# Kernel optimization log

Measured on AMD Instinct MI355X. Metric: run time of the kernel, lower is better.

Reference implementation:

```python
import jax, jax.numpy as jnp
import numpy as np

N = 10000   # nodes
E = 320000  # edges
D = 3000    # input genes
H1, H2 = 1024, 128
F1, F2, F3, F4 = 256, 512, 1024, 2048
BN_EPS = 1e-5

def setup_inputs() -> dict:
    key = jax.random.key(0)
    ks = jax.random.split(key, 30)
    rn = lambda k, s, sc=0.05: jax.random.normal(k, s, dtype=jnp.float32) * sc
    inp = {}
    inp["x"] = jax.random.normal(ks[0], (N, D), dtype=jnp.float32)
    inp["edge_w"] = jax.random.uniform(ks[1], (E,), dtype=jnp.float32)
    inp["W1"] = rn(ks[2], (D, H1))
    inp["W2"] = rn(ks[3], (H1, H2))
    inp["W3"] = rn(ks[4], (H1, H2))
    dims = [(H2, F1), (F1, F2), (F2, F3), (F3, F4), (F4, D)]
    for i, (di, do) in enumerate(dims, start=1):
        inp[f"fc{i}_w"] = rn(ks[4 + i], (di, do))
        inp[f"fc{i}_b"] = jnp.zeros((do,), jnp.float32)
        if i <= 4:
            inp[f"bn{i}_g"] = jnp.ones((do,), jnp.float32)
            inp[f"bn{i}_b"] = jnp.zeros((do,), jnp.float32)
    inp["edge_src"] = jax.random.randint(ks[20], (E,), 0, N)
    inp["edge_dst"] = jax.random.randint(ks[21], (E,), 0, N)
    return inp

def reference(x, edge_w, W1, W2, W3,
              fc1_w, fc1_b, bn1_g, bn1_b,
              fc2_w, fc2_b, bn2_g, bn2_b,
              fc3_w, fc3_b, bn3_g, bn3_b,
              fc4_w, fc4_b, bn4_g, bn4_b,
              fc5_w, fc5_b, edge_src, edge_dst):
    # sparse adjacency matmul: out[dst] += w * h[src]
    def spmm(h):
        return jax.ops.segment_sum(h[edge_src] * edge_w[:, None], edge_dst, num_segments=N)
    # GCN encoder: GraphConvolution = act(adj @ (x @ W)) (dropout inactive in eval)
    h1 = jax.nn.relu(spmm(x @ W1))
    mu = spmm(h1 @ W2)
    logvar = spmm(h1 @ W3)
    z = mu  # eval-mode reparameterize returns mu
    # inner-product adjacency decoder (act = identity)
    adj_rec = z @ z.T
    # FC stack: Linear -> BatchNorm(eval, running mean=0, var=1) -> ReLU
    inv = 1.0 / jnp.sqrt(jnp.float32(1.0 + BN_EPS))
    def fc(h, w, b, g, be):
        return jax.nn.relu((h @ w + b) * inv * g + be)
    o = fc(z, fc1_w, fc1_b, bn1_g, bn1_b)
    o = fc(o, fc2_w, fc2_b, bn2_g, bn2_b)
    o = fc(o, fc3_w, fc3_b, bn3_g, bn3_b)
    o = fc(o, fc4_w, fc4_b, bn4_g, bn4_b)
    x_rec = o @ fc5_w + fc5_b  # fc5: no batchnorm, identity act
    return (adj_rec, mu, logvar, z, x_rec)
```

## Files before the change

### kernel.cpp

```cpp
#include <hip/hip_runtime.h>
#include <stdint.h>

typedef unsigned short ushort_t;
typedef __attribute__((ext_vector_type(8))) short short8;
typedef __attribute__((ext_vector_type(4))) float f32x4;

#define N_NODES 10000
#define MP      10240
#define E_EDGES 320000
#define D_IN    3000
#define K1P     3008
#define H1      1024
#define H2      128

static __device__ __forceinline__ float b2f(ushort_t u) {
  union { uint32_t u; float f; } x; x.u = ((uint32_t)u) << 16; return x.f;
}
static __device__ __forceinline__ ushort_t f2b(float f) {
  union { float f; uint32_t u; } x; x.f = f;
  uint32_t r = x.u + 0x7FFF + ((x.u >> 16) & 1);
  return (ushort_t)(r >> 16);
}

static __device__ __forceinline__ void gload16(const void* g, void* l) {
  __builtin_amdgcn_global_load_lds(
      (const __attribute__((address_space(1))) uint32_t*)g,
      (__attribute__((address_space(3))) uint32_t*)l, 16, 0, 0);
}

__global__ void zero_k(int* p, int n) {
  int i = blockIdx.x * 256 + threadIdx.x;
  if (i < n) p[i] = 0;
}
__global__ void count_k(const int* __restrict__ ed, int* __restrict__ cnt) {
  int e = blockIdx.x * 256 + threadIdx.x;
  if (e < E_EDGES) atomicAdd(&cnt[ed[e]], 1);
}
__global__ void scan_k(const int* __restrict__ cnt, int* __restrict__ rs, int* __restrict__ cur) {
  __shared__ int sums[256];
  int t = threadIdx.x;
  const int per = 40;
  int base = t * per;
  int s = 0;
  for (int i = 0; i < per; i++) { int idx = base + i; if (idx < N_NODES) s += cnt[idx]; }
  sums[t] = s;
  __syncthreads();
  if (t == 0) { int run = 0; for (int i = 0; i < 256; i++) { int v = sums[i]; sums[i] = run; run += v; } }
  __syncthreads();
  int run = sums[t];
  for (int i = 0; i < per; i++) {
    int idx = base + i;
    if (idx < N_NODES) { rs[idx] = run; cur[idx] = run; run += cnt[idx]; }
  }
  if (t == 255) rs[N_NODES] = run;
}
__global__ void fill_k(const int* __restrict__ es, const int* __restrict__ ed,
                       const float* __restrict__ ew,
                       int* __restrict__ cur, int* __restrict__ psrc, float* __restrict__ pw) {
  int e = blockIdx.x * 256 + threadIdx.x;
  if (e >= E_EDGES) return;
  int d = ed[e];
  int pos = atomicAdd(&cur[d], 1);
  psrc[pos] = es[e];
  pw[pos] = ew[e];
}

__global__ void conv_x_k(const float* __restrict__ x, ushort_t* __restrict__ xb) {
  int g = blockIdx.x * 256 + threadIdx.x;
  int row = g / 376;
  int c8 = (g % 376) * 8;
  float v[8];
  if (row < N_NODES && c8 < 3000) {
    const float4 f0 = *(const float4*)(x + (size_t)row * 3000 + c8);
    const float4 f1 = *(const float4*)(x + (size_t)row * 3000 + c8 + 4);
    v[0]=f0.x; v[1]=f0.y; v[2]=f0.z; v[3]=f0.w;
    v[4]=f1.x; v[5]=f1.y; v[6]=f1.z; v[7]=f1.w;
  } else {
#pragma unroll
    for (int i = 0; i < 8; i++) v[i] = 0.f;
  }
  uint32_t o0 = (uint32_t)f2b(v[0]) | ((uint32_t)f2b(v[1]) << 16);
  uint32_t o1 = (uint32_t)f2b(v[2]) | ((uint32_t)f2b(v[3]) << 16);
  uint32_t o2 = (uint32_t)f2b(v[4]) | ((uint32_t)f2b(v[5]) << 16);
  uint32_t o3 = (uint32_t)f2b(v[6]) | ((uint32_t)f2b(v[7]) << 16);
  uint4 ov; ov.x=o0; ov.y=o1; ov.z=o2; ov.w=o3;
  *(uint4*)&xb[(size_t)row * K1P + c8] = ov;
}

struct Seg { const float* src; ushort_t* dst; int K, Nn, Kp, Np, tilesN, blk0; };
struct SegPack { Seg s[8]; };
__global__ void conv_w_all_k(SegPack P) {
  __shared__ float tile[32][33];
  int b = blockIdx.x;
  int si = 0;
#pragma unroll
  for (int i = 1; i < 8; ++i) if (b >= P.s[i].blk0) si = i;
  Seg sg = P.s[si];
  int rel = b - sg.blk0;
  int tk = rel / sg.tilesN, tn = rel % sg.tilesN;
  int tx = threadIdx.x & 31, ty0 = threadIdx.x >> 5;
#pragma unroll
  for (int i = 0; i < 4; ++i) {
    int ty = ty0 + i * 8;
    int k = tk * 32 + ty, n = tn * 32 + tx;
    tile[ty][tx] = (k < sg.K && n < sg.Nn) ? sg.src[(size_t)k * sg.Nn + n] : 0.f;
  }
  __syncthreads();
#pragma unroll
  for (int i = 0; i < 4; ++i) {
    int ty = ty0 + i * 8;
    int n = tn * 32 + ty, k = tk * 32 + tx;
    sg.dst[(size_t)n * sg.Kp + k] = f2b(tile[tx][ty]);
  }
}

template<int EPI>
__global__ __launch_bounds__(256)
void gemm_bt(const ushort_t* __restrict__ A, const ushort_t* __restrict__ BT, int K,
             void* __restrict__ outp, int ldOut, int realM, int realN,
             const float* __restrict__ bias, const float* __restrict__ bng,
             const float* __restrict__ bnb)
{
  __shared__ ushort_t lA[128 * 32];
  __shared__ ushort_t lB[128 * 32];
  const int tid  = threadIdx.x;
  const int row0 = blockIdx.x * 128;
  const int col0 = blockIdx.y * 128;
  const int lane = tid & 63;
  const int wave = tid >> 6;
  const int wr = (wave >> 1) * 64, wc = (wave & 1) * 64;
  const int fr = lane & 15, fq = lane >> 4;

  f32x4 acc[4][4] = {};

  const int rA = tid >> 2;
  const int cA = (tid & 3) * 8;
  const ushort_t* Ab = A  + (size_t)(row0 + rA) * K + cA;
  const ushort_t* Bb = BT + (size_t)(col0 + rA) * K + cA;
  ushort_t* lA0 = &lA[tid * 8];
  ushort_t* lA1 = &lA[2048 + tid * 8];
  ushort_t* lB0 = &lB[tid * 8];
  ushort_t* lB1 = &lB[2048 + tid * 8];
  const size_t rstep = (size_t)64 * K;

  for (int k0 = 0; k0 < K; k0 += 32) {
    gload16(Ab + k0,         lA0);
    gload16(Ab + rstep + k0, lA1);
    gload16(Bb + k0,         lB0);
    gload16(Bb + rstep + k0, lB1);
    __syncthreads();
    short8 af[4], bv[4];
#pragma unroll
    for (int m = 0; m < 4; m++) af[m] = *(const short8*)&lA[(wr + m * 16 + fr) * 32 + fq * 8];
#pragma unroll
    for (int n = 0; n < 4; n++) bv[n] = *(const short8*)&lB[(wc + n * 16 + fr) * 32 + fq * 8];
#pragma unroll
    for (int m = 0; m < 4; m++)
#pragma unroll
      for (int n = 0; n < 4; n++)
        acc[m][n] = __builtin_amdgcn_mfma_f32_16x16x32_bf16(af[m], bv[n], acc[m][n], 0, 0, 0);
    __syncthreads();
  }

  const float inv = 0.9999950000374997f;
#pragma unroll
  for (int n = 0; n < 4; n++) {
    int col = col0 + wc + n * 16 + fr;
    float s = 0.f, t = 0.f, bb = 0.f;
    if (EPI == 1) { s = inv * bng[col]; t = bias[col] * s + bnb[col]; }
    if (EPI == 2) { bb = (col < realN) ? bias[col] : 0.f; }
#pragma unroll
    for (int m = 0; m < 4; m++) {
      int rowb = row0 + wr + m * 16 + fq * 4;
#pragma unroll
      for (int r = 0; r < 4; r++) {
        int row = rowb + r;
        float v = acc[m][n][r];
        if (EPI == 0) {
          ((ushort_t*)outp)[(size_t)row * ldOut + col] = f2b(v);
        } else if (EPI == 1) {
          v = fmaxf(v * s + t, 0.f);
          ((ushort_t*)outp)[(size_t)row * ldOut + col] = f2b(v);
        } else if (EPI == 2) {
          if (row < realM && col < realN)
            ((float*)outp)[(size_t)row * ldOut + col] = v + bb;
        } else {
          if (row < realM && col < realN)
            ((float*)outp)[(size_t)row * ldOut + col] = v;
        }
      }
    }
  }
}

template<int WM, int WN, int MR, int NR, int EPI, int MINW>
__global__ __launch_bounds__(WM * WN * 64, MINW)
void gemm_p(const ushort_t* __restrict__ A, const ushort_t* __restrict__ BT, int K,
            void* __restrict__ outp, int ldOut, int realM, int realN,
            const float* __restrict__ bias, const float* __restrict__ bng,
            const float* __restrict__ bnb)
{
  constexpr int T   = WM * WN * 64;
  constexpr int BM  = WM * MR * 16;
  constexpr int BN  = WN * NR * 16;
  constexpr int ALD = (BM * 32) / (T * 8);
  constexpr int BLD = (BN * 32) / (T * 8);
  constexpr int NVM = 2 * (ALD + BLD);
  __shared__ ushort_t lA[3 * BM * 32];
  __shared__ ushort_t lB[3 * BN * 32];

  const int tid  = threadIdx.x;
  const int wave = tid >> 6;
  const int wm = wave / WN, wn = wave % WN;
  const int fr = tid & 15, fq = (tid >> 4) & 3;
  const int row0 = blockIdx.x * BM;
  const int col0 = blockIdx.y * BN;

  f32x4 acc[MR][NR] = {};

  auto stA = [&](int p, int kt, int r) {
    int c = r * T + tid;
    int row = c >> 2, slot = c & 3;
    int ss = slot ^ ((row >> 1) & 3);
    gload16(A + (size_t)(row0 + row) * K + kt * 32 + ss * 8,
            &lA[p * (BM * 32) + c * 8]);
  };
  auto stB = [&](int p, int kt, int r) {
    int c = r * T + tid;
    int row = c >> 2, slot = c & 3;
    int ss = slot ^ ((row >> 1) & 3);
    gload16(BT + (size_t)(col0 + row) * K + kt * 32 + ss * 8,
            &lB[p * (BN * 32) + c * 8]);
  };

  const int NT = K >> 5;
#pragma unroll
  for (int r = 0; r < ALD; ++r) stA(0, 0, r);
#pragma unroll
  for (int r = 0; r < BLD; ++r) stB(0, 0, r);
#pragma unroll
  for (int r = 0; r < ALD; ++r) stA(1, 1, r);
#pragma unroll
  for (int r = 0; r < BLD; ++r) stB(1, 1, r);

  for (int t = 0; t < NT; ++t) {
    const int p = t % 3;
    const int s = (t + 2) % 3;
    const int ts = (t + 2 < NT) ? t + 2 : NT - 1;
#pragma unroll
    for (int r = 0; r < ALD; ++r) stA(s, ts, r);
#pragma unroll
    for (int r = 0; r < BLD; ++r) stB(s, ts, r);
    if constexpr (NVM == 6) asm volatile("s_waitcnt vmcnt(6)" ::: "memory");
    else                    asm volatile("s_waitcnt vmcnt(8)" ::: "memory");
    asm volatile("" ::: "memory");
    __builtin_amdgcn_s_barrier();
    asm volatile("" ::: "memory");

    short8 bf[NR];
#pragma unroll
    for (int n = 0; n < NR; ++n) {
      int rb = wn * (NR * 16) + n * 16 + fr;
      bf[n] = *(const short8*)&lB[p * (BN * 32) + rb * 32 + ((fq ^ ((rb >> 1) & 3)) * 8)];
    }
    {
      short8 af[MR / 2];
#pragma unroll
      for (int m = 0; m < MR / 2; ++m) {
        int ra = wm * (MR * 16) + m * 16 + fr;
        af[m] = *(const short8*)&lA[p * (BM * 32) + ra * 32 + ((fq ^ ((ra >> 1) & 3)) * 8)];
      }
      __builtin_amdgcn_s_setprio(1);
#pragma unroll
      for (int m = 0; m < MR / 2; ++m)
#pragma unroll
        for (int n = 0; n < NR; ++n)
          acc[m][n] = __builtin_amdgcn_mfma_f32_16x16x32_bf16(af[m], bf[n], acc[m][n], 0, 0, 0);
      __builtin_amdgcn_s_setprio(0);
    }
    {
      short8 af[MR - MR / 2];
#pragma unroll
      for (int m = 0; m < MR - MR / 2; ++m) {
        int ra = wm * (MR * 16) + (m + MR / 2) * 16 + fr;
        af[m] = *(const short8*)&lA[p * (BM * 32) + ra * 32 + ((fq ^ ((ra >> 1) & 3)) * 8)];
      }
      __builtin_amdgcn_s_setprio(1);
#pragma unroll
      for (int m = 0; m < MR - MR / 2; ++m)
#pragma unroll
        for (int n = 0; n < NR; ++n)
          acc[m + MR / 2][n] = __builtin_amdgcn_mfma_f32_16x16x32_bf16(af[m], bf[n], acc[m + MR / 2][n], 0, 0, 0);
      __builtin_amdgcn_s_setprio(0);
    }
    asm volatile("" ::: "memory");
    __builtin_amdgcn_s_barrier();
    asm volatile("" ::: "memory");
  }

  const float inv = 0.9999950000374997f;
#pragma unroll
  for (int n = 0; n < NR; ++n) {
    int col = col0 + wn * (NR * 16) + n * 16 + fr;
    float s = 0.f, t = 0.f, bb = 0.f;
    if (EPI == 1) { s = inv * bng[col]; t = bias[col] * s + bnb[col]; }
    if (EPI == 2) { bb = (col < realN) ? bias[col] : 0.f; }
#pragma unroll
    for (int m = 0; m < MR; ++m) {
      int rowb = row0 + wm * (MR * 16) + m * 16 + fq * 4;
#pragma unroll
      for (int r = 0; r < 4; ++r) {
        int row = rowb + r;
        float v = acc[m][n][r];
        if (EPI == 0) {
          ((ushort_t*)outp)[(size_t)row * ldOut + col] = f2b(v);
        } else if (EPI == 1) {
          v = fmaxf(v * s + t, 0.f);
          ((ushort_t*)outp)[(size_t)row * ldOut + col] = f2b(v);
        } else if (EPI == 2) {
          if (row < realM && col < realN)
            ((float*)outp)[(size_t)row * ldOut + col] = v + bb;
        } else {
          if (row < realM && col < realN)
            ((float*)outp)[(size_t)row * ldOut + col] = v;
        }
      }
    }
  }
}

__global__ void spmm1_k(const ushort_t* __restrict__ h, ushort_t* __restrict__ o,
                        const int* __restrict__ rs, const int* __restrict__ psrc,
                        const float* __restrict__ pw) {
  int dst = blockIdx.x;
  int t = threadIdx.x;
  float a0 = 0.f, a1 = 0.f, a2 = 0.f, a3 = 0.f;
  if (dst < N_NODES) {
    int s0 = rs[dst], e0 = rs[dst + 1];
    for (int i = s0; i < e0; ++i) {
      float wv = pw[i];
      uint2 v = *(const uint2*)&h[(size_t)psrc[i] * H1 + t * 4];
      a0 += wv * b2f((ushort_t)(v.x & 0xffff));
      a1 += wv * b2f((ushort_t)(v.x >> 16));
      a2 += wv * b2f((ushort_t)(v.y & 0xffff));
      a3 += wv * b2f((ushort_t)(v.y >> 16));
    }
  }
  uint2 ov;
  ov.x = (uint32_t)f2b(fmaxf(a0, 0.f)) | ((uint32_t)f2b(fmaxf(a1, 0.f)) << 16);
  ov.y = (uint32_t)f2b(fmaxf(a2, 0.f)) | ((uint32_t)f2b(fmaxf(a3, 0.f)) << 16);
  *(uint2*)&o[(size_t)dst * H1 + t * 4] = ov;
}
__global__ void spmm2_k(const ushort_t* __restrict__ pre, float* __restrict__ mu,
                        float* __restrict__ lv, float* __restrict__ zf,
                        ushort_t* __restrict__ zb,
                        const int* __restrict__ rs, const int* __restrict__ psrc,
                        const float* __restrict__ pw) {
  int dst = blockIdx.x;
  int t = threadIdx.x;
  float acc = 0.f;
  if (dst < N_NODES) {
    int s = rs[dst], e = rs[dst + 1];
    for (int i = s; i < e; i++)
      acc += pw[i] * b2f(pre[(size_t)psrc[i] * 256 + t]);
  }
  if (t < 128) {
    zb[(size_t)dst * 128 + t] = f2b(acc);
    if (dst < N_NODES) {
      mu[(size_t)dst * 128 + t] = acc;
      zf[(size_t)dst * 128 + t] = acc;
    }
  } else if (dst < N_NODES) {
    lv[(size_t)dst * 128 + (t - 128)] = acc;
  }
}

extern "C" void kernel_launch(void* const* d_in, const int* in_sizes, int n_in,
                              void* d_out, int out_size, void* d_ws, size_t ws_size,
                              hipStream_t stream) {
  (void)in_sizes; (void)n_in; (void)out_size; (void)ws_size;
  const float* x  = (const float*)d_in[0];
  const float* ew = (const float*)d_in[1];
  const float* W1 = (const float*)d_in[2];
  const float* W2 = (const float*)d_in[3];
  const float* W3 = (const float*)d_in[4];
  const float* fc_w[5] = {(const float*)d_in[5], (const float*)d_in[9],  (const float*)d_in[13], (const float*)d_in[17], (const float*)d_in[21]};
  const float* fc_b[5] = {(const float*)d_in[6], (const float*)d_in[10], (const float*)d_in[14], (const float*)d_in[18], (const float*)d_in[22]};
  const float* bn_g[4] = {(const float*)d_in[7], (const float*)d_in[11], (const float*)d_in[15], (const float*)d_in[19]};
  const float* bn_b[4] = {(const float*)d_in[8], (const float*)d_in[12], (const float*)d_in[16], (const float*)d_in[20]};
  const int* esrc = (const int*)d_in[23];
  const int* edst = (const int*)d_in[24];
  float* out = (float*)d_out;

  float* out_adj = out;
  float* out_mu  = out + (size_t)100000000;
  float* out_lv  = out + (size_t)101280000;
  float* out_z   = out + (size_t)102560000;
  float* out_xr  = out + (size_t)103840000;

  char* w = (char*)d_ws;
  size_t off = 0;
  auto alloc = [&](size_t bytes) { size_t o = off; off = (off + bytes + 255) & ~(size_t)255; return o; };
  int*      cnt  = (int*)(w + alloc(4 * N_NODES));
  int*      rs   = (int*)(w + alloc(4 * (N_NODES + 1)));
  int*      cur  = (int*)(w + alloc(4 * N_NODES));
  int*      psrc = (int*)(w + alloc(4 * E_EDGES));
  float*    pw   = (float*)(w + alloc(4 * E_EDGES));
  ushort_t* w1T  = (ushort_t*)(w + alloc((size_t)2 * 1024 * K1P));
  ushort_t* w23T = (ushort_t*)(w + alloc((size_t)2 * 256 * 1024));
  ushort_t* f1T  = (ushort_t*)(w + alloc((size_t)2 * 256 * 128));
  ushort_t* f2T  = (ushort_t*)(w + alloc((size_t)2 * 512 * 256));
  ushort_t* f3T  = (ushort_t*)(w + alloc((size_t)2 * 1024 * 512));
  ushort_t* f4T  = (ushort_t*)(w + alloc((size_t)2 * 2048 * 1024));
  ushort_t* f5T  = (ushort_t*)(w + alloc((size_t)2 * 3072 * 2048));
  ushort_t* xb   = (ushort_t*)(w + alloc((size_t)2 * MP * K1P));
  ushort_t* xw1b = (ushort_t*)(w + alloc((size_t)2 * MP * H1));
  ushort_t* h1b  = (ushort_t*)(w + alloc((size_t)2 * MP * H1));
  ushort_t* preb = (ushort_t*)(w + alloc((size_t)2 * MP * 256));
  ushort_t* zb   = (ushort_t*)(w + alloc((size_t)2 * MP * 128));
  ushort_t* act1 = xw1b;
  ushort_t* act2 = xb;
  ushort_t* act3 = h1b;
  ushort_t* act4 = xb;

  zero_k<<<(N_NODES + 255) / 256, 256, 0, stream>>>(cnt, N_NODES);
  count_k<<<(E_EDGES + 255) / 256, 256, 0, stream>>>(edst, cnt);
  scan_k<<<1, 256, 0, stream>>>(cnt, rs, cur);
  fill_k<<<(E_EDGES + 255) / 256, 256, 0, stream>>>(esrc, edst, ew, cur, psrc, pw);

  conv_x_k<<<(MP * 376) / 256, 256, 0, stream>>>(x, xb);
  {
    SegPack P;
    int b0 = 0;
    auto mk = [&](const float* s, ushort_t* d, int K, int Nn, int Kp, int Np) {
      Seg sg; sg.src = s; sg.dst = d; sg.K = K; sg.Nn = Nn; sg.Kp = Kp; sg.Np = Np;
      sg.tilesN = Np / 32; sg.blk0 = b0;
      b0 += (Kp / 32) * (Np / 32);
      return sg;
    };
    P.s[0] = mk(W1,      w1T,                       D_IN, 1024, K1P,  1024);
    P.s[1] = mk(W2,      w23T,                      1024, 128,  1024, 128);
    P.s[2] = mk(W3,      w23T + (size_t)128 * 1024, 1024, 128,  1024, 128);
    P.s[3] = mk(fc_w[0], f1T,                       128,  256,  128,  256);
    P.s[4] = mk(fc_w[1], f2T,                       256,  512,  256,  512);
    P.s[5] = mk(fc_w[2], f3T,                       512,  1024, 512,  1024);
    P.s[6] = mk(fc_w[3], f4T,                       1024, 2048, 1024, 2048);
    P.s[7] = mk(fc_w[4], f5T,                       2048, 3000, 2048, 3072);
    conv_w_all_k<<<b0, 256, 0, stream>>>(P);
  }

  dim3 blk2(256), blk5(512);
  gemm_p<4,2,4,4,0,4><<<dim3(MP / 256, 1024 / 128), blk5, 0, stream>>>(xb, w1T, K1P, xw1b, 1024, MP, 1024, nullptr, nullptr, nullptr);
  spmm1_k<<<dim3(MP), blk2, 0, stream>>>(xw1b, h1b, rs, psrc, pw);
  gemm_bt<0><<<dim3(MP / 128, 2), blk2, 0, stream>>>(h1b, w23T, 1024, preb, 256, MP, 256, nullptr, nullptr, nullptr);
  spmm2_k<<<dim3(MP), blk2, 0, stream>>>(preb, out_mu, out_lv, out_z, zb, rs, psrc, pw);
  gemm_p<2,4,8,4,3,2><<<dim3(MP / 256, MP / 256), blk5, 0, stream>>>(zb, zb, 128, out_adj, 10000, N_NODES, N_NODES, nullptr, nullptr, nullptr);
  gemm_bt<1><<<dim3(MP / 128, 2), blk2, 0, stream>>>(zb, f1T, 128, act1, 256, MP, 256, fc_b[0], bn_g[0], bn_b[0]);
  gemm_p<4,2,4,4,1,4><<<dim3(MP / 256, 512 / 128),  blk5, 0, stream>>>(act1, f2T, 256,  act2, 512,  MP, 512,  fc_b[1], bn_g[1], bn_b[1]);
  gemm_p<4,2,4,4,1,4><<<dim3(MP / 256, 1024 / 128), blk5, 0, stream>>>(act2, f3T, 512,  act3, 1024, MP, 1024, fc_b[2], bn_g[2], bn_b[2]);
  gemm_p<4,2,4,4,1,4><<<dim3(MP / 256, 2048 / 128), blk5, 0, stream>>>(act3, f4T, 1024, act4, 2048, MP, 2048, fc_b[3], bn_g[3], bn_b[3]);
  gemm_p<2,4,8,4,2,2><<<dim3(MP / 256, 3072 / 256), blk5, 0, stream>>>(act4, f5T, 2048, out_xr, 3000, N_NODES, 3000, fc_b[4], nullptr, nullptr);
}
```

Before: 858.7 us.

## Replace templated GEMM with 128x256 single-barrier kernel plus XCD-aware block swizzle

Replaces the parameterised 512-thread GEMM with a fixed 256-thread kernel using 128x256 tiles, where each wave owns a 64-column strip across all 128 rows. The loop now issues the next-stage loads after the barrier, which removes the second per-iteration barrier. Workgroups are remapped so that consecutive tiles land on the same XCD, aiming for better L2 reuse. The z@z.T decoder writes transposed float4 stores (valid because the output is symmetric), and fc2 moves to the smaller gemm_bt kernel. Register pressure goes up with 32 accumulators per wave, and the occupancy trade-off changes.

```diff
diff --git a/kernel.cpp b/kernel.cpp
--- a/kernel.cpp
+++ b/kernel.cpp
@@ -193,136 +193,118 @@
   }
 }
 
-template<int WM, int WN, int MR, int NR, int EPI, int MINW>
-__global__ __launch_bounds__(WM * WN * 64, MINW)
-void gemm_p(const ushort_t* __restrict__ A, const ushort_t* __restrict__ BT, int K,
-            void* __restrict__ outp, int ldOut, int realM, int realN,
-            const float* __restrict__ bias, const float* __restrict__ bng,
-            const float* __restrict__ bnb)
+template<int EPI>
+__global__ __launch_bounds__(256, 2)
+void gemm3(const ushort_t* __restrict__ A, const ushort_t* __restrict__ BT, int K,
+           void* __restrict__ outp, int ldOut, int realM, int realN,
+           const float* __restrict__ bias, const float* __restrict__ bng,
+           const float* __restrict__ bnb)
 {
-  constexpr int T   = WM * WN * 64;
-  constexpr int BM  = WM * MR * 16;
-  constexpr int BN  = WN * NR * 16;
-  constexpr int ALD = (BM * 32) / (T * 8);
-  constexpr int BLD = (BN * 32) / (T * 8);
-  constexpr int NVM = 2 * (ALD + BLD);
-  __shared__ ushort_t lA[3 * BM * 32];
-  __shared__ ushort_t lB[3 * BN * 32];
-
-  const int tid  = threadIdx.x;
-  const int wave = tid >> 6;
-  const int wm = wave / WN, wn = wave % WN;
-  const int fr = tid & 15, fq = (tid >> 4) & 3;
-  const int row0 = blockIdx.x * BM;
-  const int col0 = blockIdx.y * BN;
-
-  f32x4 acc[MR][NR] = {};
+  __shared__ ushort_t lA[3 * 128 * 32];
+  __shared__ ushort_t lB[3 * 256 * 32];
+  const int tid = threadIdx.x;
+  const int wn  = tid >> 6;
+  const int fr  = tid & 15, fq = (tid >> 4) & 3;
+
+  int gx = gridDim.x;
+  int nwg = gx * gridDim.y;
+  int bid = blockIdx.y * gx + blockIdx.x;
+  int q8 = nwg >> 3, r8 = nwg & 7;
+  int xcd = bid & 7, j = bid >> 3;
+  int swz = (xcd < r8 ? xcd * (q8 + 1) : r8 * (q8 + 1) + (xcd - r8) * q8) + j;
+  const int row0 = (swz % gx) * 128;
+  const int col0 = (swz / gx) * 256;
+
+  f32x4 acc[8][4] = {};
 
   auto stA = [&](int p, int kt, int r) {
-    int c = r * T + tid;
+    int c = r * 256 + tid;
     int row = c >> 2, slot = c & 3;
     int ss = slot ^ ((row >> 1) & 3);
     gload16(A + (size_t)(row0 + row) * K + kt * 32 + ss * 8,
-            &lA[p * (BM * 32) + c * 8]);
+            &lA[p * (128 * 32) + c * 8]);
   };
   auto stB = [&](int p, int kt, int r) {
-    int c = r * T + tid;
+    int c = r * 256 + tid;
     int row = c >> 2, slot = c & 3;
     int ss = slot ^ ((row >> 1) & 3);
     gload16(BT + (size_t)(col0 + row) * K + kt * 32 + ss * 8,
-            &lB[p * (BN * 32) + c * 8]);
+            &lB[p * (256 * 32) + c * 8]);
   };
+  auto stage = [&](int p, int kt) {
+    stA(p, kt, 0); stA(p, kt, 1);
+    stB(p, kt, 0); stB(p, kt, 1); stB(p, kt, 2); stB(p, kt, 3);
+  };
 
   const int NT = K >> 5;
-#pragma unroll
-  for (int r = 0; r < ALD; ++r) stA(0, 0, r);
-#pragma unroll
-  for (int r = 0; r < BLD; ++r) stB(0, 0, r);
-#pragma unroll
-  for (int r = 0; r < ALD; ++r) stA(1, 1, r);
-#pragma unroll
-  for (int r = 0; r < BLD; ++r) stB(1, 1, r);
+  stage(0, 0);
+  stage(1, 1);
 
   for (int t = 0; t < NT; ++t) {
     const int p = t % 3;
     const int s = (t + 2) % 3;
     const int ts = (t + 2 < NT) ? t + 2 : NT - 1;
-#pragma unroll
-    for (int r = 0; r < ALD; ++r) stA(s, ts, r);
-#pragma unroll
-    for (int r = 0; r < BLD; ++r) stB(s, ts, r);
-    if constexpr (NVM == 6) asm volatile("s_waitcnt vmcnt(6)" ::: "memory");
-    else                    asm volatile("s_waitcnt vmcnt(8)" ::: "memory");
-    asm volatile("" ::: "memory");
+    asm volatile("s_waitcnt vmcnt(6)" ::: "memory");
     __builtin_amdgcn_s_barrier();
     asm volatile("" ::: "memory");
-
-    short8 bf[NR];
-#pragma unroll
-    for (int n = 0; n < NR; ++n) {
-      int rb = wn * (NR * 16) + n * 16 + fr;
-      bf[n] = *(const short8*)&lB[p * (BN * 32) + rb * 32 + ((fq ^ ((rb >> 1) & 3)) * 8)];
-    }
-    {
-      short8 af[MR / 2];
-#pragma unroll
-      for (int m = 0; m < MR / 2; ++m) {
-        int ra = wm * (MR * 16) + m * 16 + fr;
-        af[m] = *(const short8*)&lA[p * (BM * 32) + ra * 32 + ((fq ^ ((ra >> 1) & 3)) * 8)];
-      }
-      __builtin_amdgcn_s_setprio(1);
-#pragma unroll
-      for (int m = 0; m < MR / 2; ++m)
-#pragma unroll
-        for (int n = 0; n < NR; ++n)
-          acc[m][n] = __builtin_amdgcn_mfma_f32_16x16x32_bf16(af[m], bf[n], acc[m][n], 0, 0, 0);
-      __builtin_amdgcn_s_setprio(0);
-    }
-    {
-      short8 af[MR - MR / 2];
-#pragma unroll
-      for (int m = 0; m < MR - MR / 2; ++m) {
-        int ra = wm * (MR * 16) + (m + MR / 2) * 16 + fr;
-        af[m] = *(const short8*)&lA[p * (BM * 32) + ra * 32 + ((fq ^ ((ra >> 1) & 3)) * 8)];
-      }
-      __builtin_amdgcn_s_setprio(1);
-#pragma unroll
-      for (int m = 0; m < MR - MR / 2; ++m)
-#pragma unroll
-        for (int n = 0; n < NR; ++n)
-          acc[m + MR / 2][n] = __builtin_amdgcn_mfma_f32_16x16x32_bf16(af[m], bf[n], acc[m + MR / 2][n], 0, 0, 0);
-      __builtin_amdgcn_s_setprio(0);
-    }
+    stage(s, ts);
+
+    short8 bf[4], af[8];
+#pragma unroll
+    for (int n = 0; n < 4; ++n) {
+      int rb = wn * 64 + n * 16 + fr;
+      bf[n] = *(const short8*)&lB[p * (256 * 32) + rb * 32 + ((fq ^ ((rb >> 1) & 3)) * 8)];
+    }
+#pragma unroll
+    for (int m = 0; m < 8; ++m) {
+      int ra = m * 16 + fr;
+      af[m] = *(const short8*)&lA[p * (128 * 32) + ra * 32 + ((fq ^ ((ra >> 1) & 3)) * 8)];
+    }
+    __builtin_amdgcn_s_setprio(1);
+#pragma unroll
+    for (int m = 0; m < 8; ++m)
+#pragma unroll
+      for (int n = 0; n < 4; ++n)
+        acc[m][n] = __builtin_amdgcn_mfma_f32_16x16x32_bf16(af[m], bf[n], acc[m][n], 0, 0, 0);
+    __builtin_amdgcn_s_setprio(0);
     asm volatile("" ::: "memory");
-    __builtin_amdgcn_s_barrier();
-    asm volatile("" ::: "memory");
   }
 
   const float inv = 0.9999950000374997f;
 #pragma unroll
-  for (int n = 0; n < NR; ++n) {
-    int col = col0 + wn * (NR * 16) + n * 16 + fr;
-    float s = 0.f, t = 0.f, bb = 0.f;
-    if (EPI == 1) { s = inv * bng[col]; t = bias[col] * s + bnb[col]; }
+  for (int n = 0; n < 4; ++n) {
+    int col = col0 + wn * 64 + n * 16 + fr;
+    float sc = 0.f, tc = 0.f, bb = 0.f;
+    if (EPI == 1) { sc = inv * bng[col]; tc = bias[col] * sc + bnb[col]; }
     if (EPI == 2) { bb = (col < realN) ? bias[col] : 0.f; }
 #pragma unroll
-    for (int m = 0; m < MR; ++m) {
-      int rowb = row0 + wm * (MR * 16) + m * 16 + fq * 4;
-#pragma unroll
-      for (int r = 0; r < 4; ++r) {
-        int row = rowb + r;
-        float v = acc[m][n][r];
-        if (EPI == 0) {
-          ((ushort_t*)outp)[(size_t)row * ldOut + col] = f2b(v);
-        } else if (EPI == 1) {
-          v = fmaxf(v * s + t, 0.f);
-          ((ushort_t*)outp)[(size_t)row * ldOut + col] = f2b(v);
-        } else if (EPI == 2) {
-          if (row < realM && col < realN)
-            ((float*)outp)[(size_t)row * ldOut + col] = v + bb;
-        } else {
-          if (row < realM && col < realN)
-            ((float*)outp)[(size_t)row * ldOut + col] = v;
+    for (int m = 0; m < 8; ++m) {
+      int rowb = row0 + m * 16 + fq * 4;
+      if (EPI == 4) {
+        if (col < realN && rowb < realM) {
+          if (rowb + 4 <= realM) {
+            float4 v4; v4.x = acc[m][n][0]; v4.y = acc[m][n][1];
+            v4.z = acc[m][n][2]; v4.w = acc[m][n][3];
+            *(float4*)((float*)outp + (size_t)col * ldOut + rowb) = v4;
+          } else {
+            for (int r = 0; r < realM - rowb; ++r)
+              ((float*)outp)[(size_t)col * ldOut + rowb + r] = acc[m][n][r];
+          }
+        }
+      } else {
+#pragma unroll
+        for (int r = 0; r < 4; ++r) {
+          int row = rowb + r;
+          float v = acc[m][n][r];
+          if (EPI == 0) {
+            ((ushort_t*)outp)[(size_t)row * ldOut + col] = f2b(v);
+          } else if (EPI == 1) {
+            v = fmaxf(v * sc + tc, 0.f);
+            ((ushort_t*)outp)[(size_t)row * ldOut + col] = f2b(v);
+          } else if (EPI == 2) {
+            if (row < realM && col < realN)
+              ((float*)outp)[(size_t)row * ldOut + col] = v + bb;
+          }
         }
       }
     }
@@ -449,15 +431,15 @@
     conv_w_all_k<<<b0, 256, 0, stream>>>(P);
   }
 
-  dim3 blk2(256), blk5(512);
-  gemm_p<4,2,4,4,0,4><<<dim3(MP / 256, 1024 / 128), blk5, 0, stream>>>(xb, w1T, K1P, xw1b, 1024, MP, 1024, nullptr, nullptr, nullptr);
+  dim3 blk2(256);
+  gemm3<0><<<dim3(MP / 128, 1024 / 256), blk2, 0, stream>>>(xb, w1T, K1P, xw1b, 1024, MP, 1024, nullptr, nullptr, nullptr);
   spmm1_k<<<dim3(MP), blk2, 0, stream>>>(xw1b, h1b, rs, psrc, pw);
   gemm_bt<0><<<dim3(MP / 128, 2), blk2, 0, stream>>>(h1b, w23T, 1024, preb, 256, MP, 256, nullptr, nullptr, nullptr);
   spmm2_k<<<dim3(MP), blk2, 0, stream>>>(preb, out_mu, out_lv, out_z, zb, rs, psrc, pw);
-  gemm_p<2,4,8,4,3,2><<<dim3(MP / 256, MP / 256), blk5, 0, stream>>>(zb, zb, 128, out_adj, 10000, N_NODES, N_NODES, nullptr, nullptr, nullptr);
-  gemm_bt<1><<<dim3(MP / 128, 2), blk2, 0, stream>>>(zb, f1T, 128, act1, 256, MP, 256, fc_b[0], bn_g[0], bn_b[0]);
-  gemm_p<4,2,4,4,1,4><<<dim3(MP / 256, 512 / 128),  blk5, 0, stream>>>(act1, f2T, 256,  act2, 512,  MP, 512,  fc_b[1], bn_g[1], bn_b[1]);
-  gemm_p<4,2,4,4,1,4><<<dim3(MP / 256, 1024 / 128), blk5, 0, stream>>>(act2, f3T, 512,  act3, 1024, MP, 1024, fc_b[2], bn_g[2], bn_b[2]);
-  gemm_p<4,2,4,4,1,4><<<dim3(MP / 256, 2048 / 128), blk5, 0, stream>>>(act3, f4T, 1024, act4, 2048, MP, 2048, fc_b[3], bn_g[3], bn_b[3]);
-  gemm_p<2,4,8,4,2,2><<<dim3(MP / 256, 3072 / 256), blk5, 0, stream>>>(act4, f5T, 2048, out_xr, 3000, N_NODES, 3000, fc_b[4], nullptr, nullptr);
-}
+  gemm3<4><<<dim3(MP / 128, MP / 256), blk2, 0, stream>>>(zb, zb, 128, out_adj, 10000, N_NODES, N_NODES, nullptr, nullptr, nullptr);
+  gemm_bt<1><<<dim3(MP / 128, 2), blk2, 0, stream>>>(zb,   f1T, 128,  act1, 256,  MP, 256,  fc_b[0], bn_g[0], bn_b[0]);
+  gemm_bt<1><<<dim3(MP / 128, 4), blk2, 0, stream>>>(act1, f2T, 256,  act2, 512,  MP, 512,  fc_b[1], bn_g[1], bn_b[1]);
+  gemm3<1><<<dim3(MP / 128, 1024 / 256), blk2, 0, stream>>>(act2, f3T, 512,  act3, 1024, MP, 1024, fc_b[2], bn_g[2], bn_b[2]);
+  gemm3<1><<<dim3(MP / 128, 2048 / 256), blk2, 0, stream>>>(act3, f4T, 1024, act4, 2048, MP, 2048, fc_b[3], bn_g[3], bn_b[3]);
+  gemm3<2><<<dim3(MP / 128, 3072 / 256), blk2, 0, stream>>>(act4, f5T, 2048, out_xr, 3000, N_NODES, 3000, fc_b[4], nullptr, nullptr);
+}
```

New measurement: 851.6 us. Within noise of the previous version (-0.8%).
